# Kernel optimization log

Measured on AMD Instinct MI355X. Metric: run time of the kernel, lower is better.

Reference implementation:

```python
import jax, jax.numpy as jnp
import numpy as np

EMBD = 512
HEADS = 8
HEAD = EMBD // HEADS


def setup_inputs() -> dict:
    key = jax.random.key(0)
    ks = jax.random.split(key, 9)
    B, M = 4, 2048
    s = 1.0 / np.sqrt(EMBD)
    inp = {
        "x": jax.random.normal(ks[0], (B, M, EMBD), dtype=jnp.float32),
        "wq": jax.random.uniform(ks[1], (EMBD, EMBD), jnp.float32, -s, s),
        "bq": jnp.zeros((EMBD,), jnp.float32),
        "wk": jax.random.uniform(ks[2], (EMBD, EMBD), jnp.float32, -s, s),
        "bk": jnp.zeros((EMBD,), jnp.float32),
        "wv": jax.random.uniform(ks[3], (EMBD, EMBD), jnp.float32, -s, s),
        "bv": jnp.zeros((EMBD,), jnp.float32),
        "wo": jax.random.uniform(ks[4], (EMBD, EMBD), jnp.float32, -s, s),
        "bo": jnp.zeros((EMBD,), jnp.float32),
        "gamma": jnp.ones((EMBD,), jnp.float32),
        "beta": jnp.zeros((EMBD,), jnp.float32),
    }
    return inp


def layer_norm(x, gamma, beta, eps=1e-5):
    mu = jnp.mean(x, axis=-1, keepdims=True)
    var = jnp.mean(jnp.square(x - mu), axis=-1, keepdims=True)
    return (x - mu) * jax.lax.rsqrt(var + eps) * gamma + beta


def reference(x, wq, bq, wk, bk, wv, bv, wo, bo, gamma, beta):
    B, M, _ = x.shape
    norm = layer_norm(x, gamma, beta)
    # projections; reshape to [B, H, M, Dh]
    def proj(w, b):
        return (norm @ w.T + b).reshape(B, M, HEADS, HEAD).transpose(0, 2, 1, 3)
    q = proj(wq, bq)
    k = proj(wk, bk)
    v = proj(wv, bv)
    scores = jnp.einsum("bhmd,bhnd->bhmn", q, k) / np.sqrt(HEAD)
    # exclude self-attention on the diagonal
    diag = jnp.eye(M, dtype=bool)
    scores = jnp.where(diag, -jnp.inf, scores)
    attn = jax.nn.softmax(scores, axis=-1)
    ctx = jnp.einsum("bhmn,bhnd->bhmd", attn, v)
    ctx = ctx.transpose(0, 2, 1, 3).reshape(B, M, EMBD)
    out = ctx @ wo.T + bo
    return (out + x, attn)
```

## Files before the change

kernel.cpp:

```cpp
#include <hip/hip_runtime.h>

#define B_   4
#define H_   8
#define M_   2048
#define D_   512
#define DH_  64

typedef short  bf16x8 __attribute__((ext_vector_type(8)));
typedef float  f32x4  __attribute__((ext_vector_type(4)));
typedef unsigned short u16x4 __attribute__((ext_vector_type(4)));

#define EXPC 0.18033688011112042f

static __device__ __forceinline__ unsigned short f2bf(float f) {
  unsigned u = __float_as_uint(f);
  u += 0x7fffu + ((u >> 16) & 1u);
  return (unsigned short)(u >> 16);
}

static __device__ __forceinline__ int swz128(int row, int byteoff) {
  return row * 128 + (byteoff ^ ((row & 7) << 4));
}

static __device__ __forceinline__ void glds16(const void* g, void* l) {
  __builtin_amdgcn_global_load_lds(
      (const __attribute__((address_space(1))) unsigned*)g,
      (__attribute__((address_space(3))) unsigned*)l, 16, 0, 0);
}

__global__ __launch_bounds__(256) void ln_kernel(
    const float* __restrict__ x, const float* __restrict__ gamma,
    const float* __restrict__ beta, unsigned short* __restrict__ xn)
{
  int row = blockIdx.x;
  int t = threadIdx.x;
  const float* xr = x + (size_t)row * D_;
  float v0 = xr[t], v1 = xr[t + 256];
  float s = v0 + v1, ss = v0 * v0 + v1 * v1;
  #pragma unroll
  for (int m = 1; m < 64; m <<= 1) {
    s  += __shfl_xor(s, m);
    ss += __shfl_xor(ss, m);
  }
  __shared__ float red[8];
  int wid = t >> 6;
  if ((t & 63) == 0) { red[wid] = s; red[wid + 4] = ss; }
  __syncthreads();
  s  = red[0] + red[1] + red[2] + red[3];
  ss = red[4] + red[5] + red[6] + red[7];
  float mu  = s * (1.0f / D_);
  float var = ss * (1.0f / D_) - mu * mu;
  float rstd = rsqrtf(var + 1e-5f);
  unsigned short* o = xn + (size_t)row * D_;
  o[t]       = f2bf((v0 - mu) * rstd * gamma[t]       + beta[t]);
  o[t + 256] = f2bf((v1 - mu) * rstd * gamma[t + 256] + beta[t + 256]);
}

__global__ __launch_bounds__(256) void cast_w_kernel(
    const float* __restrict__ wq, const float* __restrict__ wk,
    const float* __restrict__ wv, const float* __restrict__ wo,
    unsigned short* __restrict__ wqkv, unsigned short* __restrict__ wob)
{
  int i = blockIdx.x * 256 + threadIdx.x;
  wqkv[i]          = f2bf(wq[i]);
  wqkv[i + 262144] = f2bf(wk[i]);
  wqkv[i + 524288] = f2bf(wv[i]);
  wob[i]           = f2bf(wo[i]);
}

__global__ __launch_bounds__(256) void qkv_gemm(
    const unsigned short* __restrict__ xn,
    const unsigned short* __restrict__ wqkv,
    const float* __restrict__ bq, const float* __restrict__ bk,
    const float* __restrict__ bv,
    unsigned short* __restrict__ q, unsigned short* __restrict__ k,
    unsigned short* __restrict__ vT)
{
  __shared__ __align__(16) char As[128 * 128];
  __shared__ __align__(16) char Bs[128 * 128];
  const int m0 = blockIdx.x * 128;
  const int n0 = blockIdx.y * 128;
  const int t = threadIdx.x, wid = t >> 6, lane = t & 63;
  const int wr = (wid >> 1) * 64, wc = (wid & 1) * 64;
  const int cl = lane & 15, rg = lane >> 4;
  const f32x4 z4 = {0.f, 0.f, 0.f, 0.f};
  const bool isv = (n0 >= 1024);

  f32x4 acc[4][4];
  #pragma unroll
  for (int i = 0; i < 4; ++i)
    #pragma unroll
    for (int j = 0; j < 4; ++j) acc[i][j] = z4;

  for (int k0 = 0; k0 < 512; k0 += 64) {
    __syncthreads();
    #pragma unroll
    for (int i = 0; i < 4; ++i) {
      int c = t + 256 * i;
      int row = c >> 3, off = (c & 7) * 16;
      *(uint4*)(As + swz128(row, off)) =
          *(const uint4*)((const char*)(xn + (size_t)(m0 + row) * 512 + k0) + off);
      *(uint4*)(Bs + swz128(row, off)) =
          *(const uint4*)((const char*)(wqkv + (size_t)(n0 + row) * 512 + k0) + off);
    }
    __syncthreads();
    #pragma unroll
    for (int ks = 0; ks < 2; ++ks) {
      int koff = ks * 64 + rg * 16;
      bf16x8 af[4], bfr[4];
      #pragma unroll
      for (int i = 0; i < 4; ++i)
        af[i] = *(const bf16x8*)(As + swz128(wr + i * 16 + cl, koff));
      #pragma unroll
      for (int j = 0; j < 4; ++j)
        bfr[j] = *(const bf16x8*)(Bs + swz128(wc + j * 16 + cl, koff));
      if (isv) {
        #pragma unroll
        for (int i = 0; i < 4; ++i)
          #pragma unroll
          for (int j = 0; j < 4; ++j)
            acc[i][j] = __builtin_amdgcn_mfma_f32_16x16x32_bf16(af[i], bfr[j], acc[i][j], 0, 0, 0);
      } else {
        #pragma unroll
        for (int j = 0; j < 4; ++j)
          #pragma unroll
          for (int i = 0; i < 4; ++i)
            acc[j][i] = __builtin_amdgcn_mfma_f32_16x16x32_bf16(bfr[j], af[i], acc[j][i], 0, 0, 0);
      }
    }
  }

  if (isv) {
    #pragma unroll
    for (int j = 0; j < 4; ++j) {
      int n = n0 + wc + j * 16 + cl;
      int nn = n & 511;
      int h = nn >> 6, dh = nn & 63;
      float bias = bv[nn];
      #pragma unroll
      for (int i = 0; i < 4; ++i) {
        int mrow = m0 + wr + i * 16 + rg * 4;
        int b = mrow >> 11, mm = mrow & 2047;
        u16x4 u;
        #pragma unroll
        for (int r = 0; r < 4; ++r) u[r] = f2bf(acc[i][j][r] + bias);
        *(u16x4*)(vT + ((size_t)(b * H_ + h) * DH_ + dh) * M_ + mm) = u;
      }
    }
  } else {
    const int mat = n0 >> 9;
    unsigned short* dst = mat ? k : q;
    const float* bias = mat ? bk : bq;
    #pragma unroll
    for (int j = 0; j < 4; ++j) {
      int nn0 = ((n0 + wc) & 511) + j * 16 + rg * 4;
      int h = nn0 >> 6, dh = nn0 & 63;
      f32x4 b4 = *(const f32x4*)(bias + nn0);
      #pragma unroll
      for (int i = 0; i < 4; ++i) {
        int mrow = m0 + wr + i * 16 + cl;
        int b = mrow >> 11, mm = mrow & 2047;
        u16x4 u;
        #pragma unroll
        for (int r = 0; r < 4; ++r) u[r] = f2bf(acc[j][i][r] + b4[r]);
        *(u16x4*)(dst + ((size_t)(b * H_ + h) * M_ + mm) * DH_ + dh) = u;
      }
    }
  }
}

__global__ __launch_bounds__(256, 8) void psum_kernel(
    const unsigned short* __restrict__ q, const unsigned short* __restrict__ k,
    float* __restrict__ rinv)
{
  __shared__ __align__(16) char Kb[2][8192];
  const int flat = blockIdx.x;
  const int bh = (flat & 7) * 4 + ((flat >> 3) >> 5);
  const int mb = (flat >> 3) & 31;
  const int m0 = mb * 64;
  const int t = threadIdx.x, wid = t >> 6, lane = t & 63;
  const int wr = wid * 16, cl = lane & 15, rg = lane >> 4;
  const char* qb = (const char*)(q + (size_t)bh * M_ * DH_);
  const char* kb = (const char*)(k + (size_t)bh * M_ * DH_);
  const int m_g = m0 + wr + cl;
  const f32x4 z4 = {0.f, 0.f, 0.f, 0.f};

  bf16x8 qf[2];
  #pragma unroll
  for (int ks = 0; ks < 2; ++ks)
    qf[ks] = *(const bf16x8*)(qb + (size_t)m_g * 128 + ks * 64 + rg * 16);

  const int r0 = t >> 3, c0 = t & 7;
  const int ldsoff = (t & 192) * 16;
  const size_t sK0 = (size_t)r0 * 128 + ((c0 ^ (r0 & 7)) << 4);

  glds16(kb + sK0,        Kb[0] + ldsoff);
  glds16(kb + sK0 + 4096, Kb[0] + ldsoff + 4096);

  float psum = 0.f;
  int buf = 0;
  for (int nt = 0; nt < 32; ++nt) {
    __syncthreads();
    if (nt + 1 < 32) {
      const char* src = kb + (size_t)(nt + 1) * 8192;
      glds16(src + sK0,        Kb[buf ^ 1] + ldsoff);
      glds16(src + sK0 + 4096, Kb[buf ^ 1] + ldsoff + 4096);
    }
    f32x4 s[4];
    #pragma unroll
    for (int j = 0; j < 4; ++j) s[j] = z4;
    #pragma unroll
    for (int ks = 0; ks < 2; ++ks)
      #pragma unroll
      for (int j = 0; j < 4; ++j) {
        bf16x8 kf = *(const bf16x8*)(Kb[buf] + swz128(j * 16 + cl, ks * 64 + rg * 16));
        s[j] = __builtin_amdgcn_mfma_f32_16x16x32_bf16(kf, qf[ks], s[j], 0, 0, 0);
      }
    if (nt == mb) {
      #pragma unroll
      for (int j = 0; j < 4; ++j)
        #pragma unroll
        for (int r = 0; r < 4; ++r) {
          int n_g = nt * 64 + j * 16 + rg * 4 + r;
          float p = __builtin_amdgcn_exp2f(s[j][r] * EXPC);
          psum += (n_g == m_g) ? 0.f : p;
        }
    } else {
      #pragma unroll
      for (int j = 0; j < 4; ++j)
        #pragma unroll
        for (int r = 0; r < 4; ++r)
          psum += __builtin_amdgcn_exp2f(s[j][r] * EXPC);
    }
    buf ^= 1;
  }
  psum += __shfl_xor(psum, 16);
  psum += __shfl_xor(psum, 32);
  if (lane < 16) rinv[bh * M_ + m_g] = 1.0f / psum;
}

__global__ __launch_bounds__(256, 4) void attn_kernel(
    const unsigned short* __restrict__ q,
    const unsigned short* __restrict__ k,
    const unsigned short* __restrict__ vT,
    const float* __restrict__ rinv,
    float* __restrict__ attn,
    unsigned short* __restrict__ ctx)
{
  __shared__ __align__(16) char Kb[2][8192];
  __shared__ __align__(16) char Vb[2][8192];
  __shared__ __align__(16) char Ps[4][2048];

  const int flat = blockIdx.x;
  const int bh = (flat & 7) * 4 + ((flat >> 3) >> 5);
  const int mb = (flat >> 3) & 31;
  const int m0 = mb * 64;
  const int t = threadIdx.x, wid = t >> 6, lane = t & 63;
  const int wr = wid * 16, cl = lane & 15, rg = lane >> 4;
  const int m_g = m0 + wr + cl;
  const f32x4 z4 = {0.f, 0.f, 0.f, 0.f};

  const char* qb = (const char*)(q  + (size_t)bh * M_ * DH_);
  const char* kb = (const char*)(k  + (size_t)bh * M_ * DH_);
  const char* vb = (const char*)(vT + (size_t)bh * DH_ * M_);
  float* ab = attn + (size_t)bh * M_ * M_;

  const float rv = rinv[bh * M_ + m_g];
  bf16x8 qf[2];
  #pragma unroll
  for (int ks = 0; ks < 2; ++ks)
    qf[ks] = *(const bf16x8*)(qb + (size_t)m_g * 128 + ks * 64 + rg * 16);

  const int r0 = t >> 3, c0 = t & 7;
  const int ldsoff = (t & 192) * 16;
  const size_t sK0 = (size_t)r0 * 128 + ((c0 ^ (r0 & 7)) << 4);
  const size_t sV0 = (size_t)r0 * (M_ * 2) + ((c0 ^ (r0 & 7)) << 4);

  glds16(kb + sK0,                    Kb[0] + ldsoff);
  glds16(kb + sK0 + 4096,             Kb[0] + ldsoff + 4096);
  glds16(vb + sV0,                    Vb[0] + ldsoff);
  glds16(vb + sV0 + 32 * (M_ * 2),    Vb[0] + ldsoff + 4096);

  f32x4 oc[4];
  #pragma unroll
  for (int j = 0; j < 4; ++j) oc[j] = z4;

  const int srow = lane >> 4;
  const int sch  = lane & 15;

  int buf = 0;
  for (int nt = 0; nt < 32; ++nt) {
    __syncthreads();
    if (nt + 1 < 32) {
      const char* srcK = kb + (size_t)(nt + 1) * 8192;
      const char* srcV = vb + (size_t)(nt + 1) * 128;
      glds16(srcK + sK0,                 Kb[buf ^ 1] + ldsoff);
      glds16(srcK + sK0 + 4096,          Kb[buf ^ 1] + ldsoff + 4096);
      glds16(srcV + sV0,                 Vb[buf ^ 1] + ldsoff);
      glds16(srcV + sV0 + 32 * (M_ * 2), Vb[buf ^ 1] + ldsoff + 4096);
    }
    f32x4 s[4];
    #pragma unroll
    for (int j = 0; j < 4; ++j) s[j] = z4;
    #pragma unroll
    for (int ks = 0; ks < 2; ++ks)
      #pragma unroll
      for (int j = 0; j < 4; ++j) {
        bf16x8 kf = *(const bf16x8*)(Kb[buf] + swz128(j * 16 + cl, ks * 64 + rg * 16));
        s[j] = __builtin_amdgcn_mfma_f32_16x16x32_bf16(kf, qf[ks], s[j], 0, 0, 0);
      }
    const bool dtile = (nt == mb);
    #pragma unroll
    for (int j = 0; j < 4; ++j) {
      u16x4 u;
      #pragma unroll
      for (int r = 0; r < 4; ++r) {
        int n_g = nt * 64 + j * 16 + rg * 4 + r;
        float p = __builtin_amdgcn_exp2f(s[j][r] * EXPC) * rv;
        u[r] = f2bf((dtile && n_g == m_g) ? 0.f : p);
      }
      *(u16x4*)(Ps[wid] + swz128(cl, j * 32 + rg * 8)) = u;
    }
    {
      float* abase = ab + ((size_t)(m0 + wr + srow)) * M_ + nt * 64 + sch * 4;
      #pragma unroll
      for (int it = 0; it < 4; ++it) {
        u16x4 pu = *(const u16x4*)(Ps[wid] + swz128(it * 4 + srow, sch * 8));
        f32x4 pv;
        #pragma unroll
        for (int r = 0; r < 4; ++r) pv[r] = __uint_as_float((unsigned)pu[r] << 16);
        __builtin_nontemporal_store(pv, (f32x4*)(abase + (size_t)it * 4 * M_));
      }
    }
    #pragma unroll
    for (int ks = 0; ks < 2; ++ks) {
      bf16x8 pf = *(const bf16x8*)(Ps[wid] + swz128(cl, ks * 64 + rg * 16));
      #pragma unroll
      for (int jd = 0; jd < 4; ++jd) {
        bf16x8 vf = *(const bf16x8*)(Vb[buf] + swz128(jd * 16 + cl, ks * 64 + rg * 16));
        oc[jd] = __builtin_amdgcn_mfma_f32_16x16x32_bf16(vf, pf, oc[jd], 0, 0, 0);
      }
    }
    buf ^= 1;
  }

  int b = bh >> 3, h = bh & 7;
  unsigned short* crow = ctx + ((size_t)b * M_ + m_g) * D_ + h * DH_ + rg * 4;
  #pragma unroll
  for (int jd = 0; jd < 4; ++jd) {
    u16x4 u;
    #pragma unroll
    for (int r = 0; r < 4; ++r) u[r] = f2bf(oc[jd][r]);
    *(u16x4*)(crow + jd * 16) = u;
  }
}

__global__ __launch_bounds__(256) void out_gemm(
    const unsigned short* __restrict__ ctxb,
    const unsigned short* __restrict__ wob,
    const float* __restrict__ bo,
    const float* __restrict__ x,
    float* __restrict__ out)
{
  __shared__ __align__(16) char As[128 * 128];
  __shared__ __align__(16) char Bs[128 * 128];
  const int m0 = blockIdx.x * 128;
  const int n0 = blockIdx.y * 128;
  const int t = threadIdx.x, wid = t >> 6, lane = t & 63;
  const int wr = (wid >> 1) * 64, wc = (wid & 1) * 64;
  const int cl = lane & 15, rg = lane >> 4;
  const f32x4 z4 = {0.f, 0.f, 0.f, 0.f};

  f32x4 acc[4][4];
  #pragma unroll
  for (int j = 0; j < 4; ++j)
    #pragma unroll
    for (int i = 0; i < 4; ++i) acc[j][i] = z4;

  for (int k0 = 0; k0 < 512; k0 += 64) {
    __syncthreads();
    #pragma unroll
    for (int i = 0; i < 4; ++i) {
      int c = t + 256 * i;
      int row = c >> 3, off = (c & 7) * 16;
      *(uint4*)(As + swz128(row, off)) =
          *(const uint4*)((const char*)(ctxb + (size_t)(m0 + row) * 512 + k0) + off);
      *(uint4*)(Bs + swz128(row, off)) =
          *(const uint4*)((const char*)(wob + (size_t)(n0 + row) * 512 + k0) + off);
    }
    __syncthreads();
    #pragma unroll
    for (int ks = 0; ks < 2; ++ks) {
      int koff = ks * 64 + rg * 16;
      bf16x8 af[4], bfr[4];
      #pragma unroll
      for (int i = 0; i < 4; ++i)
        af[i] = *(const bf16x8*)(As + swz128(wr + i * 16 + cl, koff));
      #pragma unroll
      for (int j = 0; j < 4; ++j)
        bfr[j] = *(const bf16x8*)(Bs + swz128(wc + j * 16 + cl, koff));
      #pragma unroll
      for (int j = 0; j < 4; ++j)
        #pragma unroll
        for (int i = 0; i < 4; ++i)
          acc[j][i] = __builtin_amdgcn_mfma_f32_16x16x32_bf16(bfr[j], af[i], acc[j][i], 0, 0, 0);
    }
  }

  #pragma unroll
  for (int j = 0; j < 4; ++j) {
    int nb = n0 + wc + j * 16 + rg * 4;
    f32x4 bo4 = *(const f32x4*)(bo + nb);
    #pragma unroll
    for (int i = 0; i < 4; ++i) {
      int m = m0 + wr + i * 16 + cl;
      f32x4 x4 = *(const f32x4*)(x + (size_t)m * 512 + nb);
      f32x4 o;
      #pragma unroll
      for (int r = 0; r < 4; ++r) o[r] = acc[j][i][r] + bo4[r] + x4[r];
      *(f32x4*)(out + (size_t)m * 512 + nb) = o;
    }
  }
}

extern "C" void kernel_launch(void* const* d_in, const int* in_sizes, int n_in,
                              void* d_out, int out_size, void* d_ws, size_t ws_size,
                              hipStream_t stream) {
  const float* x     = (const float*)d_in[0];
  const float* wq    = (const float*)d_in[1];
  const float* bq    = (const float*)d_in[2];
  const float* wk    = (const float*)d_in[3];
  const float* bk    = (const float*)d_in[4];
  const float* wv    = (const float*)d_in[5];
  const float* bv    = (const float*)d_in[6];
  const float* wo    = (const float*)d_in[7];
  const float* bo    = (const float*)d_in[8];
  const float* gamma = (const float*)d_in[9];
  const float* beta  = (const float*)d_in[10];

  char* ws = (char*)d_ws;
  unsigned short* xn   = (unsigned short*)(ws);
  unsigned short* wqkv = (unsigned short*)(ws + 8388608);
  float*          rinv = (float*)(ws + 8388608);
  unsigned short* wob  = (unsigned short*)(ws + 9961472);
  unsigned short* qb   = (unsigned short*)(ws + 10485760);
  unsigned short* kb   = (unsigned short*)(ws + 18874368);
  unsigned short* vT   = (unsigned short*)(ws + 27262976);
  unsigned short* ctx  = (unsigned short*)(ws + 35651584);

  float* out  = (float*)d_out;
  float* attn = (float*)d_out + 4194304;

  ln_kernel<<<8192, 256, 0, stream>>>(x, gamma, beta, xn);
  cast_w_kernel<<<1024, 256, 0, stream>>>(wq, wk, wv, wo, wqkv, wob);
  qkv_gemm<<<dim3(64, 12), 256, 0, stream>>>(xn, wqkv, bq, bk, bv, qb, kb, vT);
  psum_kernel<<<1024, 256, 0, stream>>>(qb, kb, rinv);
  attn_kernel<<<1024, 256, 0, stream>>>(qb, kb, vT, rinv, attn, ctx);
  out_gemm<<<dim3(64, 4), 256, 0, stream>>>(ctx, wob, bo, x, out);
}
```

Before: 215.8 us.

## Stage GEMM tiles via direct global-to-LDS loads and relax attention barrier waits

The QKV and output GEMMs now fill their shared-memory tiles with global_load_lds direct-to-LDS copies instead of loading into registers and then storing to LDS. The attention loop moves its barrier to the end of each iteration and uses an explicit s_waitcnt vmcnt(4). That wait lets the four attn-matrix stores of the current tile stay in flight while still making sure the next K/V prefetch has landed. The goal is less register traffic in the GEMMs and less stalling on outstanding stores in the attention loop. The risk is that the hand-written vmcnt accounting is fragile if the compiler reorders or adds memory operations.

```diff
diff --git a/kernel.cpp b/kernel.cpp
--- a/kernel.cpp
+++ b/kernel.cpp
@@ -26,6 +26,16 @@
   __builtin_amdgcn_global_load_lds(
       (const __attribute__((address_space(1))) unsigned*)g,
       (__attribute__((address_space(3))) unsigned*)l, 16, 0, 0);
+}
+
+static __device__ __forceinline__ void stage_tile(
+    const char* g0, size_t rstride, char* lds, int t) {
+  const int r0 = t >> 3, c0 = t & 7;
+  const char* src = g0 + (size_t)r0 * rstride + ((c0 ^ (r0 & 7)) << 4);
+  char* dst = lds + ((t & 192) << 4);
+  #pragma unroll
+  for (int c = 0; c < 4; ++c)
+    glds16(src + (size_t)c * 32 * rstride, dst + c * 4096);
 }
 
 __global__ __launch_bounds__(256) void ln_kernel(
@@ -86,6 +96,9 @@
   const f32x4 z4 = {0.f, 0.f, 0.f, 0.f};
   const bool isv = (n0 >= 1024);
 
+  const char* agb = (const char*)xn   + (size_t)m0 * 1024;
+  const char* bgb = (const char*)wqkv + (size_t)n0 * 1024;
+
   f32x4 acc[4][4];
   #pragma unroll
   for (int i = 0; i < 4; ++i)
@@ -94,15 +107,8 @@
 
   for (int k0 = 0; k0 < 512; k0 += 64) {
     __syncthreads();
-    #pragma unroll
-    for (int i = 0; i < 4; ++i) {
-      int c = t + 256 * i;
-      int row = c >> 3, off = (c & 7) * 16;
-      *(uint4*)(As + swz128(row, off)) =
-          *(const uint4*)((const char*)(xn + (size_t)(m0 + row) * 512 + k0) + off);
-      *(uint4*)(Bs + swz128(row, off)) =
-          *(const uint4*)((const char*)(wqkv + (size_t)(n0 + row) * 512 + k0) + off);
-    }
+    stage_tile(agb + k0 * 2, 1024, As, t);
+    stage_tile(bgb + k0 * 2, 1024, Bs, t);
     __syncthreads();
     #pragma unroll
     for (int ks = 0; ks < 2; ++ks) {
@@ -280,6 +286,7 @@
   glds16(kb + sK0 + 4096,             Kb[0] + ldsoff + 4096);
   glds16(vb + sV0,                    Vb[0] + ldsoff);
   glds16(vb + sV0 + 32 * (M_ * 2),    Vb[0] + ldsoff + 4096);
+  __syncthreads();
 
   f32x4 oc[4];
   #pragma unroll
@@ -290,7 +297,6 @@
 
   int buf = 0;
   for (int nt = 0; nt < 32; ++nt) {
-    __syncthreads();
     if (nt + 1 < 32) {
       const char* srcK = kb + (size_t)(nt + 1) * 8192;
       const char* srcV = vb + (size_t)(nt + 1) * 128;
@@ -340,6 +346,10 @@
         bf16x8 vf = *(const bf16x8*)(Vb[buf] + swz128(jd * 16 + cl, ks * 64 + rg * 16));
         oc[jd] = __builtin_amdgcn_mfma_f32_16x16x32_bf16(vf, pf, oc[jd], 0, 0, 0);
       }
+    }
+    if (nt + 1 < 32) {
+      asm volatile("s_waitcnt vmcnt(4) lgkmcnt(0)" ::: "memory");
+      __builtin_amdgcn_s_barrier();
     }
     buf ^= 1;
   }
@@ -371,6 +381,9 @@
   const int cl = lane & 15, rg = lane >> 4;
   const f32x4 z4 = {0.f, 0.f, 0.f, 0.f};
 
+  const char* agb = (const char*)ctxb + (size_t)m0 * 1024;
+  const char* bgb = (const char*)wob  + (size_t)n0 * 1024;
+
   f32x4 acc[4][4];
   #pragma unroll
   for (int j = 0; j < 4; ++j)
@@ -379,15 +392,8 @@
 
   for (int k0 = 0; k0 < 512; k0 += 64) {
     __syncthreads();
-    #pragma unroll
-    for (int i = 0; i < 4; ++i) {
-      int c = t + 256 * i;
-      int row = c >> 3, off = (c & 7) * 16;
-      *(uint4*)(As + swz128(row, off)) =
-          *(const uint4*)((const char*)(ctxb + (size_t)(m0 + row) * 512 + k0) + off);
-      *(uint4*)(Bs + swz128(row, off)) =
-          *(const uint4*)((const char*)(wob + (size_t)(n0 + row) * 512 + k0) + off);
-    }
+    stage_tile(agb + k0 * 2, 1024, As, t);
+    stage_tile(bgb + k0 * 2, 1024, Bs, t);
     __syncthreads();
     #pragma unroll
     for (int ks = 0; ks < 2; ++ks) {
```

New measurement: 214.1 us. Within noise of the previous version (-0.8%).
